# Kernel optimization log

Hardware: AMD Instinct MI355X
Metric: run time of the kernel (lower is better)

## Reference

```python
import jax, jax.numpy as jnp
import numpy as np

T, A, E, N, W, HID, FD = 4096, 1024, 512, 32768, 10, 150, 20
GI = 2 * A + E  # 2560
BINS = jnp.array([1, 2, 3, 4, 8, 16, 32, 64], dtype=jnp.int32)


def _mlp(x, W1, b1, W2, b2, W3, b3):
    # Score module: Linear->ReLU->Linear->ReLU->Linear->1 (dropout is a no-op in eval)
    h = jax.nn.relu(x @ W1 + b1)
    h = jax.nn.relu(h @ W2 + b2)
    return h @ W3 + b3


def setup_inputs() -> dict:
    key = jax.random.key(0)
    ks = jax.random.split(key, 20)
    s = 0.02
    inp = {
        "states": jax.random.normal(ks[0], (T, A), jnp.float32),
        "embeds": jax.random.normal(ks[1], (T, E), jnp.float32),
        "span_starts": jax.random.randint(ks[2], (N,), 0, T - W, jnp.int32),
        "span_widths": jax.random.randint(ks[3], (N,), 1, W + 1, jnp.int32),
        # attention Score params (input A)
        "Wa1": jax.random.normal(ks[4], (A, HID)) * s, "ba1": jnp.zeros((HID,)),
        "Wa2": jax.random.normal(ks[5], (HID, HID)) * s, "ba2": jnp.zeros((HID,)),
        "Wa3": jax.random.normal(ks[6], (HID, 1)) * s, "ba3": jnp.zeros((1,)),
        # width Feature embedding table: len(bins)+1 = 9 rows
        "width_emb": jax.random.normal(ks[7], (9, FD)) * s,
        # mention Score params (input GI + FD)
        "Ws1": jax.random.normal(ks[8], (GI + FD, HID)) * s, "bs1": jnp.zeros((HID,)),
        "Ws2": jax.random.normal(ks[9], (HID, HID)) * s, "bs2": jnp.zeros((HID,)),
        "Ws3": jax.random.normal(ks[10], (HID, 1)) * s, "bs3": jnp.zeros((1,)),
    }
    return inp


def reference(states, embeds, span_starts, span_widths,
              Wa1, ba1, Wa2, ba2, Wa3, ba3, width_emb,
              Ws1, bs1, Ws2, bs2, Ws3, bs3):
    # per-token attention logits  [T]
    attns = _mlp(states, Wa1, ba1, Wa2, ba2, Wa3, ba3).squeeze(-1)
    offs = jnp.arange(W)                                   # [W]
    pos = span_starts[:, None] + offs[None, :]             # [N, W]
    mask = offs[None, :] < span_widths[:, None]            # ragged span mask
    pos_c = jnp.clip(pos, 0, T - 1)
    logit = jnp.where(mask, attns[pos_c], -jnp.inf)        # [N, W]
    w = jax.nn.softmax(logit, axis=1)                      # per-span softmax
    attn_sum = jnp.einsum('nw,nwe->ne', w, embeds[pos_c])  # [N, E]
    ends = span_starts + span_widths - 1
    bin_idx = jnp.sum(span_widths[:, None] >= BINS[None, :], axis=1)
    size = width_emb[bin_idx]                              # [N, FD]
    g = jnp.concatenate([states[span_starts], states[ends], attn_sum, size], axis=1)
    scores = _mlp(g, Ws1, bs1, Ws2, bs2, Ws3, bs3).squeeze(-1)  # [N]
    return scores
```

## Files before the change

### kernel.cpp

```cpp
#include <hip/hip_runtime.h>
#include <math.h>

#define T_TOK 4096
#define A_DIM 1024
#define E_DIM 512
#define N_SPAN 32768
#define W_MAX 10
#define HID 150
#define FD 20

#define PR  160
#define KP2 160

#define WS_ATTNS 0
#define WS_PB    4096
#define WS_WPACK 1314816
#define WS_SB    1627856
#define WS_EB    3725008
#define PB_P0 0
#define PB_P1 655360
#define PB_P2 1310720
#define PB_P3 1966080
#define WP_ST  0
#define WP_V   491520
#define WP_A2  573440
#define WP_S2  599040
#define WP_WE1 624640
#define WP_TOTAL 626080
#define SB_PIECES 524288
#define EB_PIECES 262144
#define PK_ITEMS (WP_TOTAL + SB_PIECES + EB_PIECES)

typedef short  bf16x8 __attribute__((ext_vector_type(8)));
typedef float  f32x4  __attribute__((ext_vector_type(4)));

__device__ __forceinline__ float4 ld4(const float* p) { return *(const float4*)p; }

__device__ __forceinline__ unsigned short f2bf(float f) {
    unsigned u = __float_as_uint(f);
    unsigned r = u + 0x7fffu + ((u >> 16) & 1u);
    return (unsigned short)(r >> 16);
}
__device__ __forceinline__ float bf2f(short s) {
    return __uint_as_float(((unsigned)(unsigned short)s) << 16);
}
__device__ __forceinline__ bf16x8 cvt_frag(const float* p) {
    float4 u = ld4(p), v = ld4(p + 4);
    bf16x8 f;
    f[0] = (short)f2bf(u.x); f[1] = (short)f2bf(u.y);
    f[2] = (short)f2bf(u.z); f[3] = (short)f2bf(u.w);
    f[4] = (short)f2bf(v.x); f[5] = (short)f2bf(v.y);
    f[6] = (short)f2bf(v.z); f[7] = (short)f2bf(v.w);
    return f;
}

__global__ __launch_bounds__(256) void prepack_kernel(
    const float* __restrict__ states, const float* __restrict__ embeds,
    const float* __restrict__ Wa1, const float* __restrict__ Ws1,
    const float* __restrict__ Wa2, const float* __restrict__ Ws2,
    const float* __restrict__ width_emb,
    unsigned short* __restrict__ wp, unsigned short* __restrict__ Sb,
    unsigned short* __restrict__ Eb)
{
    int idx = blockIdx.x * 256 + threadIdx.x;
    if (idx >= PK_ITEMS) return;
    if (idx < WP_TOTAL) {
        float v = 0.f;
        if (idx < WP_V) {
            int gidx = idx / 163840, r = idx % 163840;
            int ngrp = r / 81920, r2 = r % 81920;
            int c = r2 / 2560, d = r2 % 2560;
            int n = d >> 5, qsw = (d >> 3) & 3, off = d & 7;
            int q = qsw ^ ((n >> 1) & 3);
            int k = c * 32 + q * 8 + off;
            int gn = ngrp * 80 + n;
            const float* W = (gidx == 0) ? Wa1 : Ws1 + (size_t)(gidx - 1) * 1024 * HID;
            if (gn < HID) v = W[(size_t)k * HID + gn];
        } else if (idx < WP_A2) {
            int r = idx - WP_V;
            int ngrp = r / 40960, r2 = r % 40960;
            int c = r2 / 2560, d = r2 % 2560;
            int n = d >> 5, qsw = (d >> 3) & 3, off = d & 7;
            int q = qsw ^ ((n >> 1) & 3);
            int k = c * 32 + q * 8 + off;
            int gn = ngrp * 80 + n;
            if (gn < HID) v = Ws1[(size_t)(2048 + k) * HID + gn];
        } else if (idx < WP_S2) {
            int e = idx - WP_A2;
            int n = e / KP2, k = e % KP2;
            if (n < HID && k < HID) v = Wa2[(size_t)k * HID + n];
        } else if (idx < WP_WE1) {
            int e = idx - WP_S2;
            int n = e / KP2, k = e % KP2;
            if (n < HID && k < HID) v = Ws2[(size_t)k * HID + n];
        } else {
            int e = idx - WP_WE1;
            int b = e / KP2, n = e % KP2;
            if (n < HID)
                for (int k = 0; k < FD; ++k)
                    v = fmaf(width_emb[b * FD + k], Ws1[(size_t)(2560 + k) * HID + n], v);
        }
        wp[idx] = f2bf(v);
    } else if (idx < WP_TOTAL + SB_PIECES) {
        int p = idx - WP_TOTAL;
        int mb = p >> 11, r = p & 2047;
        int c = r >> 6, d8 = r & 63;
        int m = d8 >> 2, qsw = d8 & 3;
        int q = qsw ^ ((m >> 1) & 3);
        const float* src = states + (size_t)(mb * 16 + m) * A_DIM + c * 32 + q * 8;
        *(bf16x8*)(Sb + (size_t)p * 8) = cvt_frag(src);
    } else {
        int p = idx - WP_TOTAL - SB_PIECES;
        int mb = p >> 10, r = p & 1023;
        int c = r >> 6, d8 = r & 63;
        int m = d8 >> 2, qsw = d8 & 3;
        int q = qsw ^ ((m >> 1) & 3);
        const float* src = embeds + (size_t)(mb * 16 + m) * E_DIM + c * 32 + q * 8;
        *(bf16x8*)(Eb + (size_t)p * 8) = cvt_frag(src);
    }
}

template<int NC, int ATILE>
__device__ __forceinline__ void gemm_m64(
    const unsigned short* __restrict__ pA,
    const unsigned short* __restrict__ pB,
    f32x4 (&acc)[4][5])
{
    bf16x8 a[2][4], bb[2][5];
#define LDC(c, s) { _Pragma("unroll") \
        for (int mt = 0; mt < 4; ++mt) \
            a[s][mt] = *(const bf16x8*)(pA + (size_t)mt * ATILE + (size_t)(c) * 512); \
        _Pragma("unroll") \
        for (int t = 0; t < 5; ++t) \
            bb[s][t] = *(const bf16x8*)(pB + (size_t)(c) * 2560 + t * 512); }
    LDC(0, 0);
#pragma unroll
    for (int c = 0; c < NC; ++c) {
        const int s = c & 1;
        if (c + 1 < NC) LDC(c + 1, s ^ 1);
#pragma unroll
        for (int mt = 0; mt < 4; ++mt)
#pragma unroll
            for (int t = 0; t < 5; ++t)
                acc[mt][t] = __builtin_amdgcn_mfma_f32_16x16x32_bf16(
                                 a[s][mt], bb[s][t], acc[mt][t], 0, 0, 0);
    }
#undef LDC
}

__global__ __launch_bounds__(64) void token_kernel(
    const unsigned short* __restrict__ Sb, const unsigned short* __restrict__ Eb,
    const unsigned short* __restrict__ wp, unsigned short* __restrict__ Pb)
{
    const int lane = threadIdx.x, l15 = lane & 15, quad = lane >> 4;
    const int bl = l15 * 32 + ((quad ^ ((l15 >> 1) & 3)) * 8);
    const int b = blockIdx.x;

    f32x4 acc[4][5];
#pragma unroll
    for (int mt = 0; mt < 4; ++mt)
#pragma unroll
        for (int t = 0; t < 5; ++t)
#pragma unroll
            for (int i = 0; i < 4; ++i) acc[mt][t][i] = 0.f;

    int mg, gidx, ngrp;
    if (b < 384) {
        const int x = b & 7, r = b >> 3;
        const int s = r % 6, g = r / 6;
        mg = g * 8 + x; gidx = s >> 1; ngrp = s & 1;
        const unsigned short* pA = Sb + (size_t)mg * 4 * 16384 + bl;
        const unsigned short* pB = wp + WP_ST + gidx * 163840 + ngrp * 81920 + bl;
        gemm_m64<32, 16384>(pA, pB, acc);
    } else {
        const int e = b - 384;
        const int x = e & 7, r = e >> 3;
        const int s = r & 1, g = r >> 1;
        mg = g * 8 + x; gidx = 3; ngrp = s;
        const unsigned short* pA = Eb + (size_t)mg * 4 * 8192 + bl;
        const unsigned short* pB = wp + WP_V + ngrp * 40960 + bl;
        gemm_m64<16, 8192>(pA, pB, acc);
    }

    unsigned short* Pg = Pb + (size_t)gidx * 655360;
#pragma unroll
    for (int mt = 0; mt < 4; ++mt)
#pragma unroll
        for (int t = 0; t < 5; ++t) {
            const int col = ngrp * 80 + t * 16 + l15;
#pragma unroll
            for (int i = 0; i < 4; ++i)
                Pg[(size_t)(mg * 64 + mt * 16 + quad * 4 + i) * PR + col] =
                    (col < HID) ? f2bf(acc[mt][t][i]) : (unsigned short)0;
        }
}

__global__ __launch_bounds__(64) void attn_tail_kernel(
    const unsigned short* __restrict__ P0, const float* __restrict__ ba1,
    const unsigned short* __restrict__ wp, const float* __restrict__ ba2,
    const float* __restrict__ Wa3, const float* __restrict__ ba3,
    float* __restrict__ attns)
{
    const int t0 = blockIdx.x * 16;
    const int lane = threadIdx.x, l15 = lane & 15, quad = lane >> 4;

    f32x4 acc[10];
#pragma unroll
    for (int nt = 0; nt < 10; ++nt)
#pragma unroll
        for (int i = 0; i < 4; ++i) acc[nt][i] = 0.f;

    const unsigned short* prow = P0 + (size_t)(t0 + l15) * PR;
    const unsigned short* bb = wp + WP_A2 + l15 * KP2 + quad * 8;

#pragma unroll
    for (int c = 0; c < 5; ++c) {
        const int k0 = c * 32;
        const int kk = k0 + quad * 8;
        bf16x8 raw = *(const bf16x8*)(prow + kk);
        bf16x8 af;
#pragma unroll
        for (int j = 0; j < 8; ++j) {
            const float b = (kk + j < HID) ? ba1[kk + j] : 0.f;
            af[j] = (short)f2bf(fmaxf(bf2f(raw[j]) + b, 0.f));
        }
#pragma unroll
        for (int nt = 0; nt < 10; ++nt) {
            bf16x8 bf = *(const bf16x8*)(bb + nt * 16 * KP2 + k0);
            acc[nt] = __builtin_amdgcn_mfma_f32_16x16x32_bf16(af, bf, acc[nt], 0, 0, 0);
        }
    }

    float sc[4] = {0.f, 0.f, 0.f, 0.f};
#pragma unroll
    for (int nt = 0; nt < 10; ++nt) {
        const int col = nt * 16 + l15;
        const float w3 = (col < HID) ? Wa3[col] : 0.f;
        const float b2 = (col < HID) ? ba2[col] : 0.f;
#pragma unroll
        for (int i = 0; i < 4; ++i)
            sc[i] = fmaf(fmaxf(acc[nt][i] + b2, 0.f), w3, sc[i]);
    }
#pragma unroll
    for (int off = 8; off >= 1; off >>= 1)
#pragma unroll
        for (int i = 0; i < 4; ++i) sc[i] += __shfl_down(sc[i], off, 16);
    if (l15 == 0) {
        const float b3 = ba3[0];
#pragma unroll
        for (int i = 0; i < 4; ++i) attns[t0 + quad * 4 + i] = sc[i] + b3;
    }
}

__global__ __launch_bounds__(256) void span_kernel(
    const unsigned short* __restrict__ Pb, const float* __restrict__ attns,
    const unsigned short* __restrict__ wp,
    const int* __restrict__ span_starts, const int* __restrict__ span_widths,
    const float* __restrict__ bs1, const float* __restrict__ bs2,
    const float* __restrict__ Ws3, const float* __restrict__ bs3,
    float* __restrict__ out)
{
    __shared__ unsigned short sHb[32][168];
    __shared__ float s_wgt[32][W_MAX];
    __shared__ int s_st[32], s_wd[32], s_bin[32], s_oid[32], s_wdr[32];
    __shared__ float sPart[4][32];
    __shared__ float sb1[KP2];

    const int tid = threadIdx.x;
    const int n0s = blockIdx.x * 32;

    if (tid < KP2) sb1[tid] = (tid < HID) ? bs1[tid] : 0.f;
    int st = 0, wd = 0;
    if (tid < 32) {
        st = span_starts[n0s + tid];
        wd = span_widths[n0s + tid];
        s_wdr[tid] = wd;
    }
    __syncthreads();
    if (tid < 32) {
        int rank = 0;
#pragma unroll
        for (int j = 0; j < 32; ++j) {
            const int wj = s_wdr[j];
            rank += (wj < wd) || (wj == wd && j < tid);
        }
        s_st[rank] = st; s_wd[rank] = wd; s_oid[rank] = tid;
        s_bin[rank] = (wd >= 1) + (wd >= 2) + (wd >= 3) + (wd >= 4) +
                      (wd >= 8) + (wd >= 16) + (wd >= 32) + (wd >= 64);
        float lg[W_MAX];
        float m = -1e30f;
#pragma unroll
        for (int w = 0; w < W_MAX; ++w)
            if (w < wd) { float a = attns[st + w]; lg[w] = a; m = fmaxf(m, a); }
        float sum = 0.f;
#pragma unroll
        for (int w = 0; w < W_MAX; ++w) {
            float e = (w < wd) ? __expf(lg[w] - m) : 0.f;
            lg[w] = e; sum += e;
        }
        float inv = 1.f / sum;
#pragma unroll
        for (int w = 0; w < W_MAX; ++w) s_wgt[rank][w] = lg[w] * inv;
    }
    __syncthreads();

    {
        const unsigned short* P1b = Pb + PB_P1;
        const unsigned short* P2b = Pb + PB_P2;
        const unsigned short* P3b = Pb + PB_P3;
        const unsigned short* WEb = wp + WP_WE1;
        const int s = tid >> 3, jl = tid & 7;
        const int sst = s_st[s], swd = s_wd[s];
        const size_t rs = (size_t)sst * PR;
        const size_t re = (size_t)(sst + swd - 1) * PR;
        const size_t rb = (size_t)s_bin[s] * PR;
        for (int c = jl; c < 20; c += 8) {
            const int j = c * 8;
            bf16x8 u1 = *(const bf16x8*)(P1b + rs + j);
            bf16x8 u2 = *(const bf16x8*)(P2b + re + j);
            bf16x8 uw = *(const bf16x8*)(WEb + rb + j);
            float acc[8];
#pragma unroll
            for (int i = 0; i < 8; ++i)
                acc[i] = bf2f(u1[i]) + bf2f(u2[i]) + bf2f(uw[i]) + sb1[j + i];
#pragma unroll
            for (int w = 0; w < W_MAX; ++w) {
                if (w < swd) {
                    float wt = s_wgt[s][w];
                    bf16x8 uv = *(const bf16x8*)(P3b + rs + (size_t)w * PR + j);
#pragma unroll
                    for (int i = 0; i < 8; ++i)
                        acc[i] = fmaf(wt, bf2f(uv[i]), acc[i]);
                }
            }
            bf16x8 pk;
#pragma unroll
            for (int i = 0; i < 8; ++i) pk[i] = (short)f2bf(fmaxf(acc[i], 0.f));
            *(bf16x8*)&sHb[s][j] = pk;
        }
    }
    __syncthreads();

    const int wv = tid >> 6, lane = tid & 63, l15 = lane & 15, quad = lane >> 4;
    const int nb = (wv < 2) ? wv * 3 : 6 + (wv - 2) * 2;
    const int cnt = (wv < 2) ? 3 : 2;

    f32x4 a2[2][3];
#pragma unroll
    for (int mt = 0; mt < 2; ++mt)
#pragma unroll
        for (int t = 0; t < 3; ++t)
#pragma unroll
            for (int i = 0; i < 4; ++i) a2[mt][t][i] = 0.f;

#pragma unroll
    for (int c = 0; c < 5; ++c) {
        int k0 = c * 32;
        bf16x8 af0 = *(const bf16x8*)&sHb[l15][k0 + quad * 8];
        bf16x8 af1 = *(const bf16x8*)&sHb[16 + l15][k0 + quad * 8];
#pragma unroll
        for (int t = 0; t < 3; ++t) {
            if (t < cnt) {
                bf16x8 b = *(const bf16x8*)(wp + WP_S2 +
                            (size_t)((nb + t) * 16 + l15) * KP2 + k0 + quad * 8);
                a2[0][t] = __builtin_amdgcn_mfma_f32_16x16x32_bf16(af0, b, a2[0][t], 0, 0, 0);
                a2[1][t] = __builtin_amdgcn_mfma_f32_16x16x32_bf16(af1, b, a2[1][t], 0, 0, 0);
            }
        }
    }

    float sc[2][4];
#pragma unroll
    for (int mt = 0; mt < 2; ++mt)
#pragma unroll
        for (int i = 0; i < 4; ++i) sc[mt][i] = 0.f;
#pragma unroll
    for (int t = 0; t < 3; ++t) {
        if (t < cnt) {
            int col = (nb + t) * 16 + l15;
            float w3 = (col < HID) ? Ws3[col] : 0.f;
            float b2 = (col < HID) ? bs2[col] : 0.f;
#pragma unroll
            for (int mt = 0; mt < 2; ++mt)
#pragma unroll
                for (int i = 0; i < 4; ++i)
                    sc[mt][i] = fmaf(fmaxf(a2[mt][t][i] + b2, 0.f), w3, sc[mt][i]);
        }
    }
#pragma unroll
    for (int off = 8; off >= 1; off >>= 1)
#pragma unroll
        for (int mt = 0; mt < 2; ++mt)
#pragma unroll
            for (int i = 0; i < 4; ++i)
                sc[mt][i] += __shfl_down(sc[mt][i], off, 16);
    if (l15 == 0) {
#pragma unroll
        for (int mt = 0; mt < 2; ++mt)
#pragma unroll
            for (int i = 0; i < 4; ++i)
                sPart[wv][mt * 16 + quad * 4 + i] = sc[mt][i];
    }
    __syncthreads();
    if (tid < 32)
        out[n0s + s_oid[tid]] = sPart[0][tid] + sPart[1][tid] + sPart[2][tid] +
                                sPart[3][tid] + bs3[0];
}

extern "C" void kernel_launch(void* const* d_in, const int* in_sizes, int n_in,
                              void* d_out, int out_size, void* d_ws, size_t ws_size,
                              hipStream_t stream)
{
    const float* states      = (const float*)d_in[0];
    const float* embeds      = (const float*)d_in[1];
    const int*   span_starts = (const int*)d_in[2];
    const int*   span_widths = (const int*)d_in[3];
    const float* Wa1 = (const float*)d_in[4];
    const float* ba1 = (const float*)d_in[5];
    const float* Wa2 = (const float*)d_in[6];
    const float* ba2 = (const float*)d_in[7];
    const float* Wa3 = (const float*)d_in[8];
    const float* ba3 = (const float*)d_in[9];
    const float* width_emb = (const float*)d_in[10];
    const float* Ws1 = (const float*)d_in[11];
    const float* bs1 = (const float*)d_in[12];
    const float* Ws2 = (const float*)d_in[13];
    const float* bs2 = (const float*)d_in[14];
    const float* Ws3 = (const float*)d_in[15];
    const float* bs3 = (const float*)d_in[16];
    float* out = (float*)d_out;

    float* ws    = (float*)d_ws;
    float* attns = ws + WS_ATTNS;
    unsigned short* Pb    = (unsigned short*)(ws + WS_PB);
    unsigned short* wpack = (unsigned short*)(ws + WS_WPACK);
    unsigned short* Sb    = (unsigned short*)(ws + WS_SB);
    unsigned short* Eb    = (unsigned short*)(ws + WS_EB);

    hipLaunchKernelGGL(prepack_kernel, dim3((PK_ITEMS + 255) / 256), dim3(256), 0, stream,
                       states, embeds, Wa1, Ws1, Wa2, Ws2, width_emb,
                       wpack, Sb, Eb);
    hipLaunchKernelGGL(token_kernel, dim3(512), dim3(64), 0, stream,
                       Sb, Eb, wpack, Pb);
    hipLaunchKernelGGL(attn_tail_kernel, dim3(T_TOK / 16), dim3(64), 0, stream,
                       Pb + PB_P0, ba1, wpack, ba2, Wa3, ba3, attns);
    hipLaunchKernelGGL(span_kernel, dim3(N_SPAN / 32), dim3(256), 0, stream,
                       Pb, attns, wpack, span_starts, span_widths,
                       bs1, bs2, Ws3, bs3, out);
}
```

Baseline: 158.4 us.

## Fuse attention MLP tail into token GEMM with 32-row two-wave tiles

Restructures the token GEMM so each block has two waves, one per 80-column half, each computing a 32-row tile. Blocks that produce the attention first-layer output apply bias and ReLU, stage the result in shared memory, and run the second and third attention MLP layers in place. This removes the separate attn_tail launch and the round trip of P0 through global memory. Each wave now does half the M work of the old version, so there are twice as many waves in flight, with less A-fragment reuse and an extra block barrier.

```diff
diff --git a/kernel.cpp b/kernel.cpp
--- a/kernel.cpp
+++ b/kernel.cpp
@@ -120,135 +120,137 @@
     }
 }
 
-template<int NC, int ATILE>
-__device__ __forceinline__ void gemm_m64(
-    const unsigned short* __restrict__ pA,
-    const unsigned short* __restrict__ pB,
-    f32x4 (&acc)[4][5])
+template<int NCH>
+__device__ __forceinline__ void gemm_reg(
+    const unsigned short* __restrict__ pA0, const unsigned short* __restrict__ pA1,
+    const unsigned short* __restrict__ pB, f32x4 (&acc)[2][5])
 {
-    bf16x8 a[2][4], bb[2][5];
-#define LDC(c, s) { _Pragma("unroll") \
-        for (int mt = 0; mt < 4; ++mt) \
-            a[s][mt] = *(const bf16x8*)(pA + (size_t)mt * ATILE + (size_t)(c) * 512); \
+    bf16x8 a0[2], a1[2], bb[2][5];
+#define LDC(c, s) { \
+        a0[s] = *(const bf16x8*)(pA0 + (size_t)(c) * 512); \
+        a1[s] = *(const bf16x8*)(pA1 + (size_t)(c) * 512); \
         _Pragma("unroll") \
         for (int t = 0; t < 5; ++t) \
             bb[s][t] = *(const bf16x8*)(pB + (size_t)(c) * 2560 + t * 512); }
     LDC(0, 0);
 #pragma unroll
-    for (int c = 0; c < NC; ++c) {
+    for (int c = 0; c < NCH; ++c) {
         const int s = c & 1;
-        if (c + 1 < NC) LDC(c + 1, s ^ 1);
-#pragma unroll
-        for (int mt = 0; mt < 4; ++mt)
-#pragma unroll
-            for (int t = 0; t < 5; ++t)
-                acc[mt][t] = __builtin_amdgcn_mfma_f32_16x16x32_bf16(
-                                 a[s][mt], bb[s][t], acc[mt][t], 0, 0, 0);
+        if (c + 1 < NCH) LDC(c + 1, s ^ 1);
+#pragma unroll
+        for (int t = 0; t < 5; ++t) {
+            acc[0][t] = __builtin_amdgcn_mfma_f32_16x16x32_bf16(a0[s], bb[s][t], acc[0][t], 0, 0, 0);
+            acc[1][t] = __builtin_amdgcn_mfma_f32_16x16x32_bf16(a1[s], bb[s][t], acc[1][t], 0, 0, 0);
+        }
     }
 #undef LDC
 }
 
-__global__ __launch_bounds__(64) void token_kernel(
+__global__ __launch_bounds__(128) void token_kernel(
     const unsigned short* __restrict__ Sb, const unsigned short* __restrict__ Eb,
-    const unsigned short* __restrict__ wp, unsigned short* __restrict__ Pb)
-{
-    const int lane = threadIdx.x, l15 = lane & 15, quad = lane >> 4;
-    const int bl = l15 * 32 + ((quad ^ ((l15 >> 1) & 3)) * 8);
-    const int b = blockIdx.x;
-
-    f32x4 acc[4][5];
-#pragma unroll
-    for (int mt = 0; mt < 4; ++mt)
-#pragma unroll
-        for (int t = 0; t < 5; ++t)
-#pragma unroll
-            for (int i = 0; i < 4; ++i) acc[mt][t][i] = 0.f;
-
-    int mg, gidx, ngrp;
-    if (b < 384) {
-        const int x = b & 7, r = b >> 3;
-        const int s = r % 6, g = r / 6;
-        mg = g * 8 + x; gidx = s >> 1; ngrp = s & 1;
-        const unsigned short* pA = Sb + (size_t)mg * 4 * 16384 + bl;
-        const unsigned short* pB = wp + WP_ST + gidx * 163840 + ngrp * 81920 + bl;
-        gemm_m64<32, 16384>(pA, pB, acc);
-    } else {
-        const int e = b - 384;
-        const int x = e & 7, r = e >> 3;
-        const int s = r & 1, g = r >> 1;
-        mg = g * 8 + x; gidx = 3; ngrp = s;
-        const unsigned short* pA = Eb + (size_t)mg * 4 * 8192 + bl;
-        const unsigned short* pB = wp + WP_V + ngrp * 40960 + bl;
-        gemm_m64<16, 8192>(pA, pB, acc);
-    }
-
-    unsigned short* Pg = Pb + (size_t)gidx * 655360;
-#pragma unroll
-    for (int mt = 0; mt < 4; ++mt)
-#pragma unroll
-        for (int t = 0; t < 5; ++t) {
-            const int col = ngrp * 80 + t * 16 + l15;
-#pragma unroll
-            for (int i = 0; i < 4; ++i)
-                Pg[(size_t)(mg * 64 + mt * 16 + quad * 4 + i) * PR + col] =
-                    (col < HID) ? f2bf(acc[mt][t][i]) : (unsigned short)0;
-        }
-}
-
-__global__ __launch_bounds__(64) void attn_tail_kernel(
-    const unsigned short* __restrict__ P0, const float* __restrict__ ba1,
-    const unsigned short* __restrict__ wp, const float* __restrict__ ba2,
+    const unsigned short* __restrict__ wp, unsigned short* __restrict__ Pb,
+    const float* __restrict__ ba1, const float* __restrict__ ba2,
     const float* __restrict__ Wa3, const float* __restrict__ ba3,
     float* __restrict__ attns)
 {
-    const int t0 = blockIdx.x * 16;
-    const int lane = threadIdx.x, l15 = lane & 15, quad = lane >> 4;
-
-    f32x4 acc[10];
-#pragma unroll
-    for (int nt = 0; nt < 10; ++nt)
-#pragma unroll
-        for (int i = 0; i < 4; ++i) acc[nt][i] = 0.f;
-
-    const unsigned short* prow = P0 + (size_t)(t0 + l15) * PR;
-    const unsigned short* bb = wp + WP_A2 + l15 * KP2 + quad * 8;
-
-#pragma unroll
-    for (int c = 0; c < 5; ++c) {
-        const int k0 = c * 32;
-        const int kk = k0 + quad * 8;
-        bf16x8 raw = *(const bf16x8*)(prow + kk);
-        bf16x8 af;
-#pragma unroll
-        for (int j = 0; j < 8; ++j) {
-            const float b = (kk + j < HID) ? ba1[kk + j] : 0.f;
-            af[j] = (short)f2bf(fmaxf(bf2f(raw[j]) + b, 0.f));
-        }
+    __shared__ __align__(16) unsigned short sHb[32][168];
+
+    const int wv = threadIdx.x >> 6;
+    const int lane = threadIdx.x & 63, l15 = lane & 15, quad = lane >> 4;
+    const int bl = l15 * 32 + ((quad ^ ((l15 >> 1) & 3)) * 8);
+    const int b = blockIdx.x;
+    const int ngrp = wv;
+
+    f32x4 acc[2][5];
+#pragma unroll
+    for (int mt = 0; mt < 2; ++mt)
+#pragma unroll
+        for (int t = 0; t < 5; ++t)
+#pragma unroll
+            for (int i = 0; i < 4; ++i) acc[mt][t][i] = 0.f;
+
+    int mb32, gidx;
+    if (b < 384) {
+        const int t = b * 2 + wv;
+        mb32 = t / 6;
+        gidx = (t % 6) >> 1;
+        const unsigned short* pA0 = Sb + (size_t)(mb32 * 2) * 16384 + bl;
+        const unsigned short* pA1 = pA0 + 16384;
+        const unsigned short* pB  = wp + WP_ST + gidx * 163840 + ngrp * 81920 + bl;
+        gemm_reg<32>(pA0, pA1, pB, acc);
+    } else {
+        mb32 = b - 384;
+        gidx = 3;
+        const unsigned short* pA0 = Eb + (size_t)(mb32 * 2) * 8192 + bl;
+        const unsigned short* pA1 = pA0 + 8192;
+        const unsigned short* pB  = wp + WP_V + ngrp * 40960 + bl;
+        gemm_reg<16>(pA0, pA1, pB, acc);
+    }
+
+    if (gidx == 0) {
+#pragma unroll
+        for (int mt = 0; mt < 2; ++mt)
+#pragma unroll
+            for (int t = 0; t < 5; ++t) {
+                const int col = ngrp * 80 + t * 16 + l15;
+                const float b1 = (col < HID) ? ba1[col] : 0.f;
+#pragma unroll
+                for (int i = 0; i < 4; ++i)
+                    sHb[mt * 16 + quad * 4 + i][col] =
+                        (col < HID) ? f2bf(fmaxf(acc[mt][t][i] + b1, 0.f))
+                                    : (unsigned short)0;
+            }
+        __syncthreads();
+        const int t0 = mb32 * 32 + wv * 16;
+        f32x4 a2[10];
+#pragma unroll
+        for (int nt = 0; nt < 10; ++nt)
+#pragma unroll
+            for (int i = 0; i < 4; ++i) a2[nt][i] = 0.f;
+
+        const unsigned short* prow = &sHb[wv * 16 + l15][0];
+        const unsigned short* bb = wp + WP_A2 + l15 * KP2 + quad * 8;
+#pragma unroll
+        for (int c = 0; c < 5; ++c) {
+            const int k0 = c * 32;
+            bf16x8 af = *(const bf16x8*)(prow + k0 + quad * 8);
+#pragma unroll
+            for (int nt = 0; nt < 10; ++nt) {
+                bf16x8 bf = *(const bf16x8*)(bb + nt * 16 * KP2 + k0);
+                a2[nt] = __builtin_amdgcn_mfma_f32_16x16x32_bf16(af, bf, a2[nt], 0, 0, 0);
+            }
+        }
+        float sc[4] = {0.f, 0.f, 0.f, 0.f};
 #pragma unroll
         for (int nt = 0; nt < 10; ++nt) {
-            bf16x8 bf = *(const bf16x8*)(bb + nt * 16 * KP2 + k0);
-            acc[nt] = __builtin_amdgcn_mfma_f32_16x16x32_bf16(af, bf, acc[nt], 0, 0, 0);
-        }
-    }
-
-    float sc[4] = {0.f, 0.f, 0.f, 0.f};
-#pragma unroll
-    for (int nt = 0; nt < 10; ++nt) {
-        const int col = nt * 16 + l15;
-        const float w3 = (col < HID) ? Wa3[col] : 0.f;
-        const float b2 = (col < HID) ? ba2[col] : 0.f;
-#pragma unroll
-        for (int i = 0; i < 4; ++i)
-            sc[i] = fmaf(fmaxf(acc[nt][i] + b2, 0.f), w3, sc[i]);
-    }
-#pragma unroll
-    for (int off = 8; off >= 1; off >>= 1)
-#pragma unroll
-        for (int i = 0; i < 4; ++i) sc[i] += __shfl_down(sc[i], off, 16);
-    if (l15 == 0) {
-        const float b3 = ba3[0];
-#pragma unroll
-        for (int i = 0; i < 4; ++i) attns[t0 + quad * 4 + i] = sc[i] + b3;
+            const int col = nt * 16 + l15;
+            const float w3 = (col < HID) ? Wa3[col] : 0.f;
+            const float b2 = (col < HID) ? ba2[col] : 0.f;
+#pragma unroll
+            for (int i = 0; i < 4; ++i)
+                sc[i] = fmaf(fmaxf(a2[nt][i] + b2, 0.f), w3, sc[i]);
+        }
+#pragma unroll
+        for (int off = 8; off >= 1; off >>= 1)
+#pragma unroll
+            for (int i = 0; i < 4; ++i) sc[i] += __shfl_down(sc[i], off, 16);
+        if (l15 == 0) {
+            const float b3 = ba3[0];
+#pragma unroll
+            for (int i = 0; i < 4; ++i) attns[t0 + quad * 4 + i] = sc[i] + b3;
+        }
+    } else {
+        unsigned short* Pg = Pb + (size_t)gidx * 655360;
+#pragma unroll
+        for (int mt = 0; mt < 2; ++mt)
+#pragma unroll
+            for (int t = 0; t < 5; ++t) {
+                const int col = ngrp * 80 + t * 16 + l15;
+#pragma unroll
+                for (int i = 0; i < 4; ++i)
+                    Pg[(size_t)(mb32 * 32 + mt * 16 + quad * 4 + i) * PR + col] =
+                        (col < HID) ? f2bf(acc[mt][t][i]) : (unsigned short)0;
+            }
     }
 }
 
@@ -440,10 +442,8 @@
     hipLaunchKernelGGL(prepack_kernel, dim3((PK_ITEMS + 255) / 256), dim3(256), 0, stream,
                        states, embeds, Wa1, Ws1, Wa2, Ws2, width_emb,
                        wpack, Sb, Eb);
-    hipLaunchKernelGGL(token_kernel, dim3(512), dim3(64), 0, stream,
-                       Sb, Eb, wpack, Pb);
-    hipLaunchKernelGGL(attn_tail_kernel, dim3(T_TOK / 16), dim3(64), 0, stream,
-                       Pb + PB_P0, ba1, wpack, ba2, Wa3, ba3, attns);
+    hipLaunchKernelGGL(token_kernel, dim3(512), dim3(128), 0, stream,
+                       Sb, Eb, wpack, Pb, ba1, ba2, Wa3, ba3, attns);
     hipLaunchKernelGGL(span_kernel, dim3(N_SPAN / 32), dim3(256), 0, stream,
                        Pb, attns, wpack, span_starts, span_widths,
                        bs1, bs2, Ws3, bs3, out);
```

New measurement: 153.7 us. 1.03x faster.
